# Kernel tuning notes

Hardware: AMD Instinct MI355X
Metric: run time of the kernel (lower is better)

## Reference

```python
import jax, jax.numpy as jnp
import numpy as np

IN_DIM = 1024
D = 2048          # feedforward_dim
G = 8             # gate_count
OUT_DIM = 1024
N = 4096
GATE_SCALE = 0.9


def setup_inputs() -> dict:
    key = jax.random.key(0)
    k = jax.random.split(key, 7)
    x = jax.random.normal(k[0], (N, IN_DIM), dtype=jnp.float32)
    gate_ids = jax.random.randint(k[1], (N, 1), 0, G)
    W1 = jax.random.normal(k[2], (2 * (1 + G) * D, IN_DIM), dtype=jnp.float32) * 0.02
    b1 = jnp.zeros((2 * (1 + G) * D,), dtype=jnp.float32)
    W2 = jax.random.normal(k[3], (D, 2 * D), dtype=jnp.float32) * 0.02
    b2 = jnp.zeros((D,), dtype=jnp.float32)
    W3 = jax.random.normal(k[4], (OUT_DIM, D), dtype=jnp.float32) * 0.02
    return {"classification_input": x, "gate_ids": gate_ids,
            "W1": W1, "b1": b1, "W2": W2, "b2": b2, "W3": W3}


def reference(classification_input, gate_ids, W1, b1, W2, b2, W3):
    n = classification_input.shape[0]
    # l1 + relu: [N, (1+G)*2D]
    h = jax.nn.relu(classification_input @ W1.T + b1)
    # mask: gate blocks scaled by 0.9, shared block (last) always on
    onehot = jax.nn.one_hot(gate_ids[:, 0], G, dtype=h.dtype) * GATE_SCALE  # [N, G]
    mask = jnp.concatenate([onehot, jnp.ones((n, 1), dtype=h.dtype)], axis=1)  # [N, G+1]
    # masked block-sum over the (1+G) blocks of size 2D
    h = h.reshape(n, 1 + G, 2 * D)
    s = jnp.einsum('ngd,ng->nd', h, mask)  # [N, 2D]
    h2 = jax.nn.relu(s @ W2.T + b2)        # [N, D]
    return h2 @ W3.T                        # [N, OUT_DIM]
```

## Files before the change

kernel.cpp:

```cpp
#include <hip/hip_runtime.h>
#include <cstdint>


#define NP 5120
#define NROWT 40
#define NROWS 4096
#define GATES 8

typedef short short8 __attribute__((ext_vector_type(8)));
typedef unsigned short ushort8v __attribute__((ext_vector_type(8)));
typedef float f32x4 __attribute__((ext_vector_type(4)));

constexpr int BM = 128, BN = 128, BK = 32;
constexpr int LDSW_FB = 40;

__device__ __forceinline__ unsigned short f2b(float f) {
    __bf16 h = (__bf16)f;
    return __builtin_bit_cast(unsigned short, h);
}

__device__ __forceinline__ void gload_lds16(const void* g, void* l) {
    __builtin_amdgcn_global_load_lds(
        (const __attribute__((address_space(1))) void*)g,
        (__attribute__((address_space(3))) void*)l, 16, 0, 0);
}


__global__ void bucket_kernel(const int* __restrict__ gid,
                              int* __restrict__ perm,
                              int* __restrict__ tile_gate,
                              unsigned short* __restrict__ zrow)
{
    __shared__ int cnt[GATES], pstart[GATES], cur[GATES];
    const int t = threadIdx.x;
    if (zrow) {
        ushort4 z; z.x = 0; z.y = 0; z.z = 0; z.w = 0;
        ((ushort4*)zrow)[t] = z;
    }
    if (t < GATES) cnt[t] = 0;
    __syncthreads();
    for (int i = t; i < NROWS; i += 256) atomicAdd(&cnt[gid[i]], 1);
    __syncthreads();
    if (t == 0) {
        int off = 0;
        for (int g = 0; g < GATES; g++) {
            pstart[g] = off;
            cur[g] = 0;
            off += (cnt[g] + 127) & ~127;
        }
    }
    __syncthreads();
    for (int i = t; i < NP; i += 256) perm[i] = -1;
    if (t < NROWT) {
        int r0 = t * 128;
        int tg = 0;
        for (int g = 0; g < GATES; g++) {
            int pc = (cnt[g] + 127) & ~127;
            if (r0 >= pstart[g] && r0 < pstart[g] + pc) tg = g;
        }
        tile_gate[t] = tg;
    }
    __syncthreads();
    for (int i = t; i < NROWS; i += 256) {
        int g = gid[i];
        int p = atomicAdd(&cur[g], 1);
        perm[pstart[g] + p] = i;
    }
}

__global__ __launch_bounds__(256)
void cast_kernel(const float* __restrict__ src, unsigned short* __restrict__ dst,
                 int n8)
{
    int i = blockIdx.x * 256 + threadIdx.x;
    const int stride = gridDim.x * 256;
    for (; i < n8; i += stride) {
        const float4* s4 = (const float4*)(src + (size_t)i * 8);
        float4 a = s4[0], b = s4[1];
        ushort8v v;
        v[0] = f2b(a.x); v[1] = f2b(a.y); v[2] = f2b(a.z); v[3] = f2b(a.w);
        v[4] = f2b(b.x); v[5] = f2b(b.y); v[6] = f2b(b.z); v[7] = f2b(b.w);
        *(ushort8v*)(dst + (size_t)i * 8) = v;
    }
}

__global__ __launch_bounds__(256, 2)
void l1_fast(const unsigned short* __restrict__ xbf,
             const unsigned short* __restrict__ W1bf,
             const float* __restrict__ b1,
             const int* __restrict__ perm,
             const int* __restrict__ tile_gate,
             unsigned short* __restrict__ s_out)
{
    __shared__ __align__(16) unsigned short As[BM][BK];
    __shared__ __align__(16) unsigned short Bg[BN][BK];
    __shared__ __align__(16) unsigned short Bs[BN][BK];

    const int t = threadIdx.x;
    const int rbase = blockIdx.y * BM;
    const int cbase = blockIdx.x * BN;
    const int gate = tile_gate[blockIdx.y];

    const int srow  = t >> 2;
    const int skcol = ((t & 3) ^ ((t >> 3) & 3)) * 8;

    int g0 = perm[rbase + srow];      if (g0 < 0) g0 = NROWS;
    int g1 = perm[rbase + srow + 64]; if (g1 < 0) g1 = NROWS;

    const unsigned short* a0 = xbf + (size_t)g0 * 1024 + skcol;
    const unsigned short* a1 = xbf + (size_t)g1 * 1024 + skcol;
    const unsigned short* bg0 = W1bf + ((size_t)(gate * 4096 + cbase + srow)) * 1024 + skcol;
    const unsigned short* bg1 = bg0 + (size_t)64 * 1024;
    const unsigned short* bs0 = W1bf + ((size_t)(GATES * 4096 + cbase + srow)) * 1024 + skcol;
    const unsigned short* bs1 = bs0 + (size_t)64 * 1024;

    const int wchunk = (t >> 6) * 1024;

    f32x4 accg[4][4], accs[4][4];
#pragma unroll
    for (int m = 0; m < 4; m++)
#pragma unroll
        for (int n = 0; n < 4; n++) {
            accg[m][n] = (f32x4){0.f, 0.f, 0.f, 0.f};
            accs[m][n] = (f32x4){0.f, 0.f, 0.f, 0.f};
        }

    const int lane = t & 63;
    const int wid  = t >> 6;
    const int wr = wid >> 1, wc = wid & 1;
    const int lr = lane & 15;
    const int kb = (((lane >> 4) ^ ((lr >> 1) & 3))) * 8;

    for (int k0 = 0; k0 < 1024; k0 += BK) {
        gload_lds16(a0 + k0,  (char*)As + wchunk);
        gload_lds16(a1 + k0,  (char*)As + wchunk + 4096);
        gload_lds16(bg0 + k0, (char*)Bg + wchunk);
        gload_lds16(bg1 + k0, (char*)Bg + wchunk + 4096);
        gload_lds16(bs0 + k0, (char*)Bs + wchunk);
        gload_lds16(bs1 + k0, (char*)Bs + wchunk + 4096);
        __syncthreads();

        short8 af[4];
#pragma unroll
        for (int m = 0; m < 4; m++)
            af[m] = *(const short8*)&As[wr * 64 + m * 16 + lr][kb];
        {
            short8 bf[4];
#pragma unroll
            for (int n = 0; n < 4; n++)
                bf[n] = *(const short8*)&Bg[wc * 64 + n * 16 + lr][kb];
#pragma unroll
            for (int m = 0; m < 4; m++)
#pragma unroll
                for (int n = 0; n < 4; n++)
                    accg[m][n] = __builtin_amdgcn_mfma_f32_16x16x32_bf16(
                        af[m], bf[n], accg[m][n], 0, 0, 0);
        }
        {
            short8 bf[4];
#pragma unroll
            for (int n = 0; n < 4; n++)
                bf[n] = *(const short8*)&Bs[wc * 64 + n * 16 + lr][kb];
#pragma unroll
            for (int m = 0; m < 4; m++)
#pragma unroll
                for (int n = 0; n < 4; n++)
                    accs[m][n] = __builtin_amdgcn_mfma_f32_16x16x32_bf16(
                        af[m], bf[n], accs[m][n], 0, 0, 0);
        }
        __syncthreads();
    }

    const int rowoff = (lane >> 4) * 4;
#pragma unroll
    for (int m = 0; m < 4; m++) {
        const int prow = rbase + wr * 64 + m * 16 + rowoff;
#pragma unroll
        for (int n = 0; n < 4; n++) {
            const int col = cbase + wc * 64 + n * 16 + lr;
            const float b1g = b1[(size_t)gate * 4096 + col];
            const float b1s = b1[(size_t)GATES * 4096 + col];
#pragma unroll
            for (int j = 0; j < 4; j++) {
                float vg = accg[m][n][j] + b1g;
                float vs = accs[m][n][j] + b1s;
                float sv = 0.9f * fmaxf(vg, 0.f) + fmaxf(vs, 0.f);
                s_out[(size_t)(prow + j) * 4096 + col] = f2b(sv);
            }
        }
    }
}

__global__ __launch_bounds__(256, 2)
void l2_fast(const unsigned short* __restrict__ s_in,
             const unsigned short* __restrict__ W2bf,
             const float* __restrict__ b2,
             unsigned short* __restrict__ h2)
{
    __shared__ __align__(16) unsigned short As[BM][BK];
    __shared__ __align__(16) unsigned short Bt[BN][BK];

    const int t = threadIdx.x;
    const int rbase = blockIdx.y * BM;
    const int cbase = blockIdx.x * BN;
    const int srow  = t >> 2;
    const int skcol = ((t & 3) ^ ((t >> 3) & 3)) * 8;

    const unsigned short* a0 = s_in + (size_t)(rbase + srow) * 4096 + skcol;
    const unsigned short* a1 = a0 + (size_t)64 * 4096;
    const unsigned short* b0 = W2bf + (size_t)(cbase + srow) * 4096 + skcol;
    const unsigned short* b1p = b0 + (size_t)64 * 4096;

    const int wchunk = (t >> 6) * 1024;

    f32x4 acc[4][4];
#pragma unroll
    for (int m = 0; m < 4; m++)
#pragma unroll
        for (int n = 0; n < 4; n++) acc[m][n] = (f32x4){0.f, 0.f, 0.f, 0.f};

    const int lane = t & 63;
    const int wid  = t >> 6;
    const int wr = wid >> 1, wc = wid & 1;
    const int lr = lane & 15;
    const int kb = (((lane >> 4) ^ ((lr >> 1) & 3))) * 8;

    for (int k0 = 0; k0 < 4096; k0 += BK) {
        gload_lds16(a0 + k0,  (char*)As + wchunk);
        gload_lds16(a1 + k0,  (char*)As + wchunk + 4096);
        gload_lds16(b0 + k0,  (char*)Bt + wchunk);
        gload_lds16(b1p + k0, (char*)Bt + wchunk + 4096);
        __syncthreads();

        short8 af[4], bf[4];
#pragma unroll
        for (int m = 0; m < 4; m++)
            af[m] = *(const short8*)&As[wr * 64 + m * 16 + lr][kb];
#pragma unroll
        for (int n = 0; n < 4; n++)
            bf[n] = *(const short8*)&Bt[wc * 64 + n * 16 + lr][kb];
#pragma unroll
        for (int m = 0; m < 4; m++)
#pragma unroll
            for (int n = 0; n < 4; n++)
                acc[m][n] = __builtin_amdgcn_mfma_f32_16x16x32_bf16(
                    af[m], bf[n], acc[m][n], 0, 0, 0);
        __syncthreads();
    }

    const int rowoff = (lane >> 4) * 4;
#pragma unroll
    for (int m = 0; m < 4; m++) {
        const int prow = rbase + wr * 64 + m * 16 + rowoff;
#pragma unroll
        for (int n = 0; n < 4; n++) {
            const int col = cbase + wc * 64 + n * 16 + lr;
            const float bb = b2[col];
#pragma unroll
            for (int j = 0; j < 4; j++) {
                float v = fmaxf(acc[m][n][j] + bb, 0.f);
                h2[(size_t)(prow + j) * 2048 + col] = f2b(v);
            }
        }
    }
}

__global__ __launch_bounds__(256, 2)
void l3_fast(const unsigned short* __restrict__ h2,
             const unsigned short* __restrict__ W3bf,
             const int* __restrict__ perm,
             float* __restrict__ out)
{
    __shared__ __align__(16) unsigned short As[BM][BK];
    __shared__ __align__(16) unsigned short Bt[BN][BK];

    const int t = threadIdx.x;
    const int rbase = blockIdx.y * BM;
    const int cbase = blockIdx.x * BN;
    const int srow  = t >> 2;
    const int skcol = ((t & 3) ^ ((t >> 3) & 3)) * 8;

    const unsigned short* a0 = h2 + (size_t)(rbase + srow) * 2048 + skcol;
    const unsigned short* a1 = a0 + (size_t)64 * 2048;
    const unsigned short* b0 = W3bf + (size_t)(cbase + srow) * 2048 + skcol;
    const unsigned short* b1p = b0 + (size_t)64 * 2048;

    const int wchunk = (t >> 6) * 1024;

    f32x4 acc[4][4];
#pragma unroll
    for (int m = 0; m < 4; m++)
#pragma unroll
        for (int n = 0; n < 4; n++) acc[m][n] = (f32x4){0.f, 0.f, 0.f, 0.f};

    const int lane = t & 63;
    const int wid  = t >> 6;
    const int wr = wid >> 1, wc = wid & 1;
    const int lr = lane & 15;
    const int kb = (((lane >> 4) ^ ((lr >> 1) & 3))) * 8;

    for (int k0 = 0; k0 < 2048; k0 += BK) {
        gload_lds16(a0 + k0,  (char*)As + wchunk);
        gload_lds16(a1 + k0,  (char*)As + wchunk + 4096);
        gload_lds16(b0 + k0,  (char*)Bt + wchunk);
        gload_lds16(b1p + k0, (char*)Bt + wchunk + 4096);
        __syncthreads();

        short8 af[4], bf[4];
#pragma unroll
        for (int m = 0; m < 4; m++)
            af[m] = *(const short8*)&As[wr * 64 + m * 16 + lr][kb];
#pragma unroll
        for (int n = 0; n < 4; n++)
            bf[n] = *(const short8*)&Bt[wc * 64 + n * 16 + lr][kb];
#pragma unroll
        for (int m = 0; m < 4; m++)
#pragma unroll
            for (int n = 0; n < 4; n++)
                acc[m][n] = __builtin_amdgcn_mfma_f32_16x16x32_bf16(
                    af[m], bf[n], acc[m][n], 0, 0, 0);
        __syncthreads();
    }

    const int rowoff = (lane >> 4) * 4;
#pragma unroll
    for (int m = 0; m < 4; m++) {
        const int prow = rbase + wr * 64 + m * 16 + rowoff;
#pragma unroll
        for (int n = 0; n < 4; n++) {
            const int col = cbase + wc * 64 + n * 16 + lr;
#pragma unroll
            for (int j = 0; j < 4; j++) {
                int orow = perm[prow + j];
                if (orow >= 0)
                    out[(size_t)orow * 1024 + col] = acc[m][n][j];
            }
        }
    }
}

__global__ __launch_bounds__(256, 2)
void l1_fb(const float* __restrict__ x, const float* __restrict__ W1,
           const float* __restrict__ b1, const int* __restrict__ perm,
           const int* __restrict__ tile_gate, unsigned short* __restrict__ s_out)
{
    __shared__ __align__(16) unsigned short As[BM][LDSW_FB];
    __shared__ __align__(16) unsigned short Bg[BN][LDSW_FB];
    __shared__ __align__(16) unsigned short Bs[BN][LDSW_FB];

    const int t = threadIdx.x;
    const int rbase = blockIdx.y * BM;
    const int cbase = blockIdx.x * BN;
    const int gate = tile_gate[blockIdx.y];
    const int srow_t = t >> 3;
    const int scol   = (t & 7) * 4;

    int grow[4];
#pragma unroll
    for (int rr = 0; rr < 4; rr++) grow[rr] = perm[rbase + rr * 32 + srow_t];

    const float* Bgp = W1 + ((size_t)gate * 4096 + cbase) * 1024;
    const float* Bsp = W1 + ((size_t)GATES * 4096 + cbase) * 1024;

    f32x4 accg[4][4], accs[4][4];
#pragma unroll
    for (int m = 0; m < 4; m++)
#pragma unroll
        for (int n = 0; n < 4; n++) {
            accg[m][n] = (f32x4){0.f, 0.f, 0.f, 0.f};
            accs[m][n] = (f32x4){0.f, 0.f, 0.f, 0.f};
        }

    const int lane = t & 63;
    const int wid  = t >> 6;
    const int wr = wid >> 1, wc = wid & 1;
    const int lr = lane & 15;
    const int kb = (lane >> 4) * 8;

    for (int k0 = 0; k0 < 1024; k0 += BK) {
        __syncthreads();
#pragma unroll
        for (int rr = 0; rr < 4; rr++) {
            const int row = rr * 32 + srow_t;
            float4 av = make_float4(0.f, 0.f, 0.f, 0.f);
            if (grow[rr] >= 0)
                av = *(const float4*)(x + (size_t)grow[rr] * 1024 + k0 + scol);
            ushort4 pa;
            pa.x = f2b(av.x); pa.y = f2b(av.y); pa.z = f2b(av.z); pa.w = f2b(av.w);
            *(ushort4*)&As[row][scol] = pa;

            float4 gv = *(const float4*)(Bgp + (size_t)row * 1024 + k0 + scol);
            ushort4 pg;
            pg.x = f2b(gv.x); pg.y = f2b(gv.y); pg.z = f2b(gv.z); pg.w = f2b(gv.w);
            *(ushort4*)&Bg[row][scol] = pg;

            float4 sv = *(const float4*)(Bsp + (size_t)row * 1024 + k0 + scol);
            ushort4 ps;
            ps.x = f2b(sv.x); ps.y = f2b(sv.y); ps.z = f2b(sv.z); ps.w = f2b(sv.w);
            *(ushort4*)&Bs[row][scol] = ps;
        }
        __syncthreads();

        short8 af[4], bgf[4], bsf[4];
#pragma unroll
        for (int m = 0; m < 4; m++)
            af[m] = *(const short8*)&As[wr * 64 + m * 16 + lr][kb];
#pragma unroll
        for (int n = 0; n < 4; n++) {
            bgf[n] = *(const short8*)&Bg[wc * 64 + n * 16 + lr][kb];
            bsf[n] = *(const short8*)&Bs[wc * 64 + n * 16 + lr][kb];
        }
#pragma unroll
        for (int m = 0; m < 4; m++)
#pragma unroll
            for (int n = 0; n < 4; n++) {
                accg[m][n] = __builtin_amdgcn_mfma_f32_16x16x32_bf16(
                    af[m], bgf[n], accg[m][n], 0, 0, 0);
                accs[m][n] = __builtin_amdgcn_mfma_f32_16x16x32_bf16(
                    af[m], bsf[n], accs[m][n], 0, 0, 0);
            }
    }

    const int rowoff = (lane >> 4) * 4;
#pragma unroll
    for (int m = 0; m < 4; m++) {
        const int prow = rbase + wr * 64 + m * 16 + rowoff;
#pragma unroll
        for (int n = 0; n < 4; n++) {
            const int col = cbase + wc * 64 + n * 16 + lr;
            const float b1g = b1[(size_t)gate * 4096 + col];
            const float b1s = b1[(size_t)GATES * 4096 + col];
#pragma unroll
            for (int j = 0; j < 4; j++) {
                float vg = accg[m][n][j] + b1g;
                float vs = accs[m][n][j] + b1s;
                float sv = 0.9f * fmaxf(vg, 0.f) + fmaxf(vs, 0.f);
                s_out[(size_t)(prow + j) * 4096 + col] = f2b(sv);
            }
        }
    }
}

__global__ __launch_bounds__(256, 2)
void l2_fb(const unsigned short* __restrict__ s_in, const float* __restrict__ W2,
           const float* __restrict__ b2, unsigned short* __restrict__ h2)
{
    __shared__ __align__(16) unsigned short As[BM][LDSW_FB];
    __shared__ __align__(16) unsigned short Bt[BN][LDSW_FB];

    const int t = threadIdx.x;
    const int rbase = blockIdx.y * BM;
    const int cbase = blockIdx.x * BN;
    const int srow_t = t >> 3;
    const int scol   = (t & 7) * 4;

    f32x4 acc[4][4];
#pragma unroll
    for (int m = 0; m < 4; m++)
#pragma unroll
        for (int n = 0; n < 4; n++) acc[m][n] = (f32x4){0.f, 0.f, 0.f, 0.f};

    const int lane = t & 63;
    const int wid  = t >> 6;
    const int wr = wid >> 1, wc = wid & 1;
    const int lr = lane & 15;
    const int kb = (lane >> 4) * 8;

    for (int k0 = 0; k0 < 4096; k0 += BK) {
        __syncthreads();
#pragma unroll
        for (int rr = 0; rr < 4; rr++) {
            const int row = rr * 32 + srow_t;
            ushort4 av = *(const ushort4*)(s_in + (size_t)(rbase + row) * 4096 + k0 + scol);
            *(ushort4*)&As[row][scol] = av;
            float4 bv = *(const float4*)(W2 + (size_t)(cbase + row) * 4096 + k0 + scol);
            ushort4 pb;
            pb.x = f2b(bv.x); pb.y = f2b(bv.y); pb.z = f2b(bv.z); pb.w = f2b(bv.w);
            *(ushort4*)&Bt[row][scol] = pb;
        }
        __syncthreads();

        short8 af[4], bf[4];
#pragma unroll
        for (int m = 0; m < 4; m++)
            af[m] = *(const short8*)&As[wr * 64 + m * 16 + lr][kb];
#pragma unroll
        for (int n = 0; n < 4; n++)
            bf[n] = *(const short8*)&Bt[wc * 64 + n * 16 + lr][kb];
#pragma unroll
        for (int m = 0; m < 4; m++)
#pragma unroll
            for (int n = 0; n < 4; n++)
                acc[m][n] = __builtin_amdgcn_mfma_f32_16x16x32_bf16(
                    af[m], bf[n], acc[m][n], 0, 0, 0);
    }

    const int rowoff = (lane >> 4) * 4;
#pragma unroll
    for (int m = 0; m < 4; m++) {
        const int prow = rbase + wr * 64 + m * 16 + rowoff;
#pragma unroll
        for (int n = 0; n < 4; n++) {
            const int col = cbase + wc * 64 + n * 16 + lr;
            const float bb = b2[col];
#pragma unroll
            for (int j = 0; j < 4; j++) {
                float v = fmaxf(acc[m][n][j] + bb, 0.f);
                h2[(size_t)(prow + j) * 2048 + col] = f2b(v);
            }
        }
    }
}

__global__ __launch_bounds__(256, 2)
void l3_fb(const unsigned short* __restrict__ h2, const float* __restrict__ W3,
           const int* __restrict__ perm, float* __restrict__ out)
{
    __shared__ __align__(16) unsigned short As[BM][LDSW_FB];
    __shared__ __align__(16) unsigned short Bt[BN][LDSW_FB];

    const int t = threadIdx.x;
    const int rbase = blockIdx.y * BM;
    const int cbase = blockIdx.x * BN;
    const int srow_t = t >> 3;
    const int scol   = (t & 7) * 4;

    f32x4 acc[4][4];
#pragma unroll
    for (int m = 0; m < 4; m++)
#pragma unroll
        for (int n = 0; n < 4; n++) acc[m][n] = (f32x4){0.f, 0.f, 0.f, 0.f};

    const int lane = t & 63;
    const int wid  = t >> 6;
    const int wr = wid >> 1, wc = wid & 1;
    const int lr = lane & 15;
    const int kb = (lane >> 4) * 8;

    for (int k0 = 0; k0 < 2048; k0 += BK) {
        __syncthreads();
#pragma unroll
        for (int rr = 0; rr < 4; rr++) {
            const int row = rr * 32 + srow_t;
            ushort4 av = *(const ushort4*)(h2 + (size_t)(rbase + row) * 2048 + k0 + scol);
            *(ushort4*)&As[row][scol] = av;
            float4 bv = *(const float4*)(W3 + (size_t)(cbase + row) * 2048 + k0 + scol);
            ushort4 pb;
            pb.x = f2b(bv.x); pb.y = f2b(bv.y); pb.z = f2b(bv.z); pb.w = f2b(bv.w);
            *(ushort4*)&Bt[row][scol] = pb;
        }
        __syncthreads();

        short8 af[4], bf[4];
#pragma unroll
        for (int m = 0; m < 4; m++)
            af[m] = *(const short8*)&As[wr * 64 + m * 16 + lr][kb];
#pragma unroll
        for (int n = 0; n < 4; n++)
            bf[n] = *(const short8*)&Bt[wc * 64 + n * 16 + lr][kb];
#pragma unroll
        for (int m = 0; m < 4; m++)
#pragma unroll
            for (int n = 0; n < 4; n++)
                acc[m][n] = __builtin_amdgcn_mfma_f32_16x16x32_bf16(
                    af[m], bf[n], acc[m][n], 0, 0, 0);
    }

    const int rowoff = (lane >> 4) * 4;
#pragma unroll
    for (int m = 0; m < 4; m++) {
        const int prow = rbase + wr * 64 + m * 16 + rowoff;
#pragma unroll
        for (int n = 0; n < 4; n++) {
            const int col = cbase + wc * 64 + n * 16 + lr;
#pragma unroll
            for (int j = 0; j < 4; j++) {
                int orow = perm[prow + j];
                if (orow >= 0)
                    out[(size_t)orow * 1024 + col] = acc[m][n][j];
            }
        }
    }
}

extern "C" void kernel_launch(void* const* d_in, const int* in_sizes, int n_in,
                              void* d_out, int out_size, void* d_ws, size_t ws_size,
                              hipStream_t stream)
{
    const float* x   = (const float*)d_in[0];
    const int*   gid = (const int*)d_in[1];
    const float* W1  = (const float*)d_in[2];
    const float* b1  = (const float*)d_in[3];
    const float* W2  = (const float*)d_in[4];
    const float* b2  = (const float*)d_in[5];
    const float* W3  = (const float*)d_in[6];
    float* out = (float*)d_out;
    char* ws = (char*)d_ws;

    auto alignup = [](size_t v) { return (v + 255) & ~(size_t)255; };

    size_t off = 0;
    const size_t perm_off = off; off = alignup(off + (size_t)NP * 4);
    const size_t tg_off   = off; off = alignup(off + (size_t)NROWT * 4);
    const size_t xbf_off  = off; off = alignup(off + (size_t)4097 * 1024 * 2);
    const size_t w1_off   = off; off = alignup(off + (size_t)36864 * 1024 * 2);
    const size_t w2_off   = off; off = alignup(off + (size_t)2048 * 4096 * 2);
    const size_t w3_off   = off; off = alignup(off + (size_t)1024 * 2048 * 2);
    const size_t sB_off   = off; off = alignup(off + (size_t)NP * 4096 * 2);
    const size_t h2B_off  = off; off = alignup(off + (size_t)NP * 2048 * 2);
    const size_t need_big = off;

    const size_t sS_off   = 32768;
    const size_t h2S_off  = sS_off + (size_t)NP * 4096 * 2;
    const size_t need_sm  = h2S_off + (size_t)NP * 2048 * 2;

    int* perm = (int*)(ws + perm_off);
    int* tile_gate = (int*)(ws + tg_off);

    if (ws_size >= need_big) {
        unsigned short* xbf  = (unsigned short*)(ws + xbf_off);
        unsigned short* w1bf = (unsigned short*)(ws + w1_off);
        unsigned short* w2bf = (unsigned short*)(ws + w2_off);
        unsigned short* w3bf = (unsigned short*)(ws + w3_off);
        unsigned short* s_perm = (unsigned short*)(ws + sB_off);
        unsigned short* h2 = (unsigned short*)(ws + h2B_off);
        unsigned short* zrow = xbf + (size_t)NROWS * 1024;

        bucket_kernel<<<1, 256, 0, stream>>>(gid, perm, tile_gate, zrow);
        cast_kernel<<<2048, 256, 0, stream>>>(x,  xbf,  (NROWS * 1024) / 8);
        cast_kernel<<<2048, 256, 0, stream>>>(W1, w1bf, (36864 * 1024) / 8);
        cast_kernel<<<2048, 256, 0, stream>>>(W2, w2bf, (2048 * 4096) / 8);
        cast_kernel<<<1024, 256, 0, stream>>>(W3, w3bf, (1024 * 2048) / 8);
        l1_fast<<<dim3(32, NROWT), 256, 0, stream>>>(xbf, w1bf, b1, perm, tile_gate, s_perm);
        l2_fast<<<dim3(16, NROWT), 256, 0, stream>>>(s_perm, w2bf, b2, h2);
        l3_fast<<<dim3(8, NROWT), 256, 0, stream>>>(h2, w3bf, perm, out);
    } else if (ws_size >= need_sm) {
        unsigned short* s_perm = (unsigned short*)(ws + sS_off);
        unsigned short* h2 = (unsigned short*)(ws + h2S_off);

        bucket_kernel<<<1, 256, 0, stream>>>(gid, perm, tile_gate, (unsigned short*)nullptr);
        l1_fb<<<dim3(32, NROWT), 256, 0, stream>>>(x, W1, b1, perm, tile_gate, s_perm);
        l2_fb<<<dim3(16, NROWT), 256, 0, stream>>>(s_perm, W2, b2, h2);
        l3_fb<<<dim3(8, NROWT), 256, 0, stream>>>(h2, W3, perm, out);
    }
}
```

Measured before the change: 542.5 us.

## Double-buffer LDS tiles in all three GEMM kernels to overlap loads with MFMA

```diff
diff --git a/kernel.cpp b/kernel.cpp
--- a/kernel.cpp
+++ b/kernel.cpp
@@ -92,9 +92,9 @@
              const int* __restrict__ tile_gate,
              unsigned short* __restrict__ s_out)
 {
-    __shared__ __align__(16) unsigned short As[BM][BK];
-    __shared__ __align__(16) unsigned short Bg[BN][BK];
-    __shared__ __align__(16) unsigned short Bs[BN][BK];
+    __shared__ __align__(16) unsigned short As[2][BM][BK];
+    __shared__ __align__(16) unsigned short Bg[2][BM][BK];
+    __shared__ __align__(16) unsigned short Bs[2][BM][BK];
 
     const int t = threadIdx.x;
     const int rbase = blockIdx.y * BM;
@@ -131,24 +131,36 @@
     const int lr = lane & 15;
     const int kb = (((lane >> 4) ^ ((lr >> 1) & 3))) * 8;
 
+    gload_lds16(a0,  (char*)As[0] + wchunk);
+    gload_lds16(a1,  (char*)As[0] + wchunk + 4096);
+    gload_lds16(bg0, (char*)Bg[0] + wchunk);
+    gload_lds16(bg1, (char*)Bg[0] + wchunk + 4096);
+    gload_lds16(bs0, (char*)Bs[0] + wchunk);
+    gload_lds16(bs1, (char*)Bs[0] + wchunk + 4096);
+    __syncthreads();
+
+    int cur = 0;
     for (int k0 = 0; k0 < 1024; k0 += BK) {
-        gload_lds16(a0 + k0,  (char*)As + wchunk);
-        gload_lds16(a1 + k0,  (char*)As + wchunk + 4096);
-        gload_lds16(bg0 + k0, (char*)Bg + wchunk);
-        gload_lds16(bg1 + k0, (char*)Bg + wchunk + 4096);
-        gload_lds16(bs0 + k0, (char*)Bs + wchunk);
-        gload_lds16(bs1 + k0, (char*)Bs + wchunk + 4096);
-        __syncthreads();
+        const int kn = k0 + BK;
+        if (kn < 1024) {
+            const int nxt = cur ^ 1;
+            gload_lds16(a0 + kn,  (char*)As[nxt] + wchunk);
+            gload_lds16(a1 + kn,  (char*)As[nxt] + wchunk + 4096);
+            gload_lds16(bg0 + kn, (char*)Bg[nxt] + wchunk);
+            gload_lds16(bg1 + kn, (char*)Bg[nxt] + wchunk + 4096);
+            gload_lds16(bs0 + kn, (char*)Bs[nxt] + wchunk);
+            gload_lds16(bs1 + kn, (char*)Bs[nxt] + wchunk + 4096);
+        }
 
         short8 af[4];
 #pragma unroll
         for (int m = 0; m < 4; m++)
-            af[m] = *(const short8*)&As[wr * 64 + m * 16 + lr][kb];
+            af[m] = *(const short8*)&As[cur][wr * 64 + m * 16 + lr][kb];
         {
             short8 bf[4];
 #pragma unroll
             for (int n = 0; n < 4; n++)
-                bf[n] = *(const short8*)&Bg[wc * 64 + n * 16 + lr][kb];
+                bf[n] = *(const short8*)&Bg[cur][wc * 64 + n * 16 + lr][kb];
 #pragma unroll
             for (int m = 0; m < 4; m++)
 #pragma unroll
@@ -160,7 +172,7 @@
             short8 bf[4];
 #pragma unroll
             for (int n = 0; n < 4; n++)
-                bf[n] = *(const short8*)&Bs[wc * 64 + n * 16 + lr][kb];
+                bf[n] = *(const short8*)&Bs[cur][wc * 64 + n * 16 + lr][kb];
 #pragma unroll
             for (int m = 0; m < 4; m++)
 #pragma unroll
@@ -169,6 +181,7 @@
                         af[m], bf[n], accs[m][n], 0, 0, 0);
         }
         __syncthreads();
+        cur ^= 1;
     }
 
     const int rowoff = (lane >> 4) * 4;
@@ -197,8 +210,8 @@
              const float* __restrict__ b2,
              unsigned short* __restrict__ h2)
 {
-    __shared__ __align__(16) unsigned short As[BM][BK];
-    __shared__ __align__(16) unsigned short Bt[BN][BK];
+    __shared__ __align__(16) unsigned short As[2][BM][BK];
+    __shared__ __align__(16) unsigned short Bt[2][BM][BK];
 
     const int t = threadIdx.x;
     const int rbase = blockIdx.y * BM;
@@ -225,20 +238,30 @@
     const int lr = lane & 15;
     const int kb = (((lane >> 4) ^ ((lr >> 1) & 3))) * 8;
 
+    gload_lds16(a0,  (char*)As[0] + wchunk);
+    gload_lds16(a1,  (char*)As[0] + wchunk + 4096);
+    gload_lds16(b0,  (char*)Bt[0] + wchunk);
+    gload_lds16(b1p, (char*)Bt[0] + wchunk + 4096);
+    __syncthreads();
+
+    int cur = 0;
     for (int k0 = 0; k0 < 4096; k0 += BK) {
-        gload_lds16(a0 + k0,  (char*)As + wchunk);
-        gload_lds16(a1 + k0,  (char*)As + wchunk + 4096);
-        gload_lds16(b0 + k0,  (char*)Bt + wchunk);
-        gload_lds16(b1p + k0, (char*)Bt + wchunk + 4096);
-        __syncthreads();
+        const int kn = k0 + BK;
+        if (kn < 4096) {
+            const int nxt = cur ^ 1;
+            gload_lds16(a0 + kn,  (char*)As[nxt] + wchunk);
+            gload_lds16(a1 + kn,  (char*)As[nxt] + wchunk + 4096);
+            gload_lds16(b0 + kn,  (char*)Bt[nxt] + wchunk);
+            gload_lds16(b1p + kn, (char*)Bt[nxt] + wchunk + 4096);
+        }
 
         short8 af[4], bf[4];
 #pragma unroll
         for (int m = 0; m < 4; m++)
-            af[m] = *(const short8*)&As[wr * 64 + m * 16 + lr][kb];
+            af[m] = *(const short8*)&As[cur][wr * 64 + m * 16 + lr][kb];
 #pragma unroll
         for (int n = 0; n < 4; n++)
-            bf[n] = *(const short8*)&Bt[wc * 64 + n * 16 + lr][kb];
+            bf[n] = *(const short8*)&Bt[cur][wc * 64 + n * 16 + lr][kb];
 #pragma unroll
         for (int m = 0; m < 4; m++)
 #pragma unroll
@@ -246,6 +269,7 @@
                 acc[m][n] = __builtin_amdgcn_mfma_f32_16x16x32_bf16(
                     af[m], bf[n], acc[m][n], 0, 0, 0);
         __syncthreads();
+        cur ^= 1;
     }
 
     const int rowoff = (lane >> 4) * 4;
@@ -271,8 +295,8 @@
              const int* __restrict__ perm,
              float* __restrict__ out)
 {
-    __shared__ __align__(16) unsigned short As[BM][BK];
-    __shared__ __align__(16) unsigned short Bt[BN][BK];
+    __shared__ __align__(16) unsigned short As[2][BM][BK];
+    __shared__ __align__(16) unsigned short Bt[2][BM][BK];
 
     const int t = threadIdx.x;
     const int rbase = blockIdx.y * BM;
@@ -299,20 +323,30 @@
     const int lr = lane & 15;
     const int kb = (((lane >> 4) ^ ((lr >> 1) & 3))) * 8;
 
+    gload_lds16(a0,  (char*)As[0] + wchunk);
+    gload_lds16(a1,  (char*)As[0] + wchunk + 4096);
+    gload_lds16(b0,  (char*)Bt[0] + wchunk);
+    gload_lds16(b1p, (char*)Bt[0] + wchunk + 4096);
+    __syncthreads();
+
+    int cur = 0;
     for (int k0 = 0; k0 < 2048; k0 += BK) {
-        gload_lds16(a0 + k0,  (char*)As + wchunk);
-        gload_lds16(a1 + k0,  (char*)As + wchunk + 4096);
-        gload_lds16(b0 + k0,  (char*)Bt + wchunk);
-        gload_lds16(b1p + k0, (char*)Bt + wchunk + 4096);
-        __syncthreads();
+        const int kn = k0 + BK;
+        if (kn < 2048) {
+            const int nxt = cur ^ 1;
+            gload_lds16(a0 + kn,  (char*)As[nxt] + wchunk);
+            gload_lds16(a1 + kn,  (char*)As[nxt] + wchunk + 4096);
+            gload_lds16(b0 + kn,  (char*)Bt[nxt] + wchunk);
+            gload_lds16(b1p + kn, (char*)Bt[nxt] + wchunk + 4096);
+        }
 
         short8 af[4], bf[4];
 #pragma unroll
         for (int m = 0; m < 4; m++)
-            af[m] = *(const short8*)&As[wr * 64 + m * 16 + lr][kb];
+            af[m] = *(const short8*)&As[cur][wr * 64 + m * 16 + lr][kb];
 #pragma unroll
         for (int n = 0; n < 4; n++)
-            bf[n] = *(const short8*)&Bt[wc * 64 + n * 16 + lr][kb];
+            bf[n] = *(const short8*)&Bt[cur][wc * 64 + n * 16 + lr][kb];
 #pragma unroll
         for (int m = 0; m < 4; m++)
 #pragma unroll
@@ -320,6 +354,7 @@
                 acc[m][n] = __builtin_amdgcn_mfma_f32_16x16x32_bf16(
                     af[m], bf[n], acc[m][n], 0, 0, 0);
         __syncthreads();
+        cur ^= 1;
     }
 
     const int rowoff = (lane >> 4) * 4;
```

Measured after the change: 561.8 us. 1.04x slower.
